# Kernel optimization log

Measured on AMD Instinct MI355X. Metric: run time of the kernel, lower is better.

Reference implementation:

```python
import jax, jax.numpy as jnp
import numpy as np

N, E, D, H = 16000, 256000, 128, 4
ALPHA = 0.2  # LeakyReLU negative slope


def setup_inputs() -> dict:
    key = jax.random.key(0)
    ks = jax.random.split(key, 9)
    s = 0.1
    return {
        "h": jax.random.normal(ks[0], (N, D), jnp.float32),
        "W": jax.random.normal(ks[1], (H, D, D), jnp.float32) * s,
        "a": jax.random.normal(ks[2], (H, 2 * D), jnp.float32) * s,
        "W_ih": jax.random.normal(ks[3], (3 * D, H * D), jnp.float32) * s,
        "W_hh": jax.random.normal(ks[4], (3 * D, D), jnp.float32) * s,
        "b_ih": jnp.zeros((3 * D,), jnp.float32),
        "b_hh": jnp.zeros((3 * D,), jnp.float32),
        "src": jax.random.randint(ks[5], (E,), 0, N, jnp.int32),
        "dst": jax.random.randint(ks[6], (E,), 0, N, jnp.int32),
    }


def reference(h, W, a, W_ih, W_hh, b_ih, b_hh, src, dst):
    n = h.shape[0]
    # Per-head linear transform: Wh[n,h,d]
    Wh = jnp.einsum("nd,hde->nhe", h, W)
    a1, a2 = a[:, :D], a[:, D:]
    s_src = jnp.einsum("nhd,hd->nh", Wh, a1)  # src attention logits
    s_dst = jnp.einsum("nhd,hd->nh", Wh, a2)  # dst attention logits
    e = jax.nn.leaky_relu(s_src[src] + s_dst[dst], ALPHA)  # [E,H]
    # Segment softmax over incoming edges of each dst node
    m = jax.ops.segment_max(e, dst, num_segments=n)          # [N,H]
    ex = jnp.exp(e - m[dst])
    denom = jax.ops.segment_sum(ex, dst, num_segments=n)     # [N,H]
    att = ex / denom[dst]                                    # [E,H]
    # Weighted message aggregation: h_prime[n,h,d]
    h_prime = jax.ops.segment_sum(att[:, :, None] * Wh[src], dst, num_segments=n)
    x = h_prime.reshape(n, H * D)  # concat heads
    # PyTorch GRUCell(input=H*D, hidden=D)
    gi = x @ W_ih.T + b_ih
    gh = h @ W_hh.T + b_hh
    i_r, i_z, i_n = jnp.split(gi, 3, axis=1)
    h_r, h_z, h_n = jnp.split(gh, 3, axis=1)
    r = jax.nn.sigmoid(i_r + h_r)
    z = jax.nn.sigmoid(i_z + h_z)
    nvec = jnp.tanh(i_n + r * h_n)
    return (1.0 - z) * nvec + z * h
```

## Files before the change

### kernel.cpp

```cpp
#include <hip/hip_runtime.h>
#include <math.h>

#define N_NODES 16000
#define E_EDGES 256000
#define DIM 128
#define HEADS 4
#define LRELU_ALPHA 0.2f
#define SLOT 64

typedef unsigned short u16;
typedef unsigned int u32;
typedef short bf16x8 __attribute__((ext_vector_type(8)));
typedef float floatx4 __attribute__((ext_vector_type(4)));

#define AS1 __attribute__((address_space(1)))
#define AS3 __attribute__((address_space(3)))

__device__ __forceinline__ u16 f2bf(float f) {
    u32 u = __float_as_uint(f);
    u32 r = (u + 0x7fffu + ((u >> 16) & 1u)) >> 16;
    return (u16)r;
}
__device__ __forceinline__ float bflo(u32 v) { return __uint_as_float(v << 16); }
__device__ __forceinline__ float bfhi(u32 v) { return __uint_as_float(v & 0xffff0000u); }
__device__ __forceinline__ u32 pack2(float lo, float hi) {
    return (u32)f2bf(lo) | ((u32)f2bf(hi) << 16);
}

__global__ __launch_bounds__(256) void prep_kernel(
    const float* __restrict__ hin, const float* __restrict__ W, const float* __restrict__ a,
    const float* __restrict__ W_ih, const float* __restrict__ W_hh,
    const int* __restrict__ src, const int* __restrict__ dst,
    u16* __restrict__ xcat, u16* __restrict__ Wihb, u16* __restrict__ Wb,
    u16* __restrict__ Wcat, float* __restrict__ wa1, float* __restrict__ wa2,
    u32* __restrict__ cnt, int* __restrict__ ssort)
{
    const int b = blockIdx.x;
    const int tid = threadIdx.x;
    if (b < 1000) {
        int e = b * 256 + tid;
        u32 base = cnt[N_NODES];
        int d = dst[e];
        u32 pos = atomicAdd(&cnt[d], 1u) - base;
        ssort[d * SLOT + pos] = src[e];
    } else if (b < 1768) {
        int i = (b - 1000) * 256 + tid;
        Wihb[i] = f2bf(W_ih[i]);
        if (i < HEADS * DIM * DIM) Wb[i] = f2bf(W[i]);
    } else if (b < 1960) {
        int t = (b - 1768) * 256 + tid;
        int jp = t >> 7, e = t & 127;
        int j = (jp < 256) ? jp : jp + 128;
        Wcat[(size_t)j * 640 + 512 + e] = f2bf(W_hh[jp * 128 + e]);
    } else if (b < 1962) {
        int t = (b - 1960) * 256 + tid;
        int h = t >> 7;
        const float* wrow = W + (long)t * DIM;
        const float* a1 = a + h * 2 * DIM;
        const float* a2 = a1 + DIM;
        float s1 = 0.f, s2 = 0.f;
        for (int e = 0; e < DIM; ++e) {
            float w = wrow[e];
            s1 = fmaf(w, a1[e], s1);
            s2 = fmaf(w, a2[e], s2);
        }
        wa1[t] = s1;
        wa2[t] = s2;
    } else {
        int p = (b - 1962) * 256 + tid;
        float2 hv = ((const float2*)hin)[p];
        ((u32*)xcat)[(p >> 6) * 320 + 256 + (p & 63)] = pack2(hv.x, hv.y);
    }
}

__device__ __forceinline__ void score_wave(int n, const float* __restrict__ hin,
    const float* __restrict__ wa1, const float* __restrict__ wa2,
    float* __restrict__ s_src, float* __restrict__ s_dst, int lane)
{
    float2 hv = ((const float2*)hin)[n * 64 + lane];
    float ps[4], qs[4];
    #pragma unroll
    for (int h = 0; h < 4; ++h) {
        float2 w1 = ((const float2*)(wa1 + h * 128))[lane];
        float2 w2 = ((const float2*)(wa2 + h * 128))[lane];
        float p = hv.x * w1.x + hv.y * w1.y;
        float q = hv.x * w2.x + hv.y * w2.y;
        #pragma unroll
        for (int off = 32; off > 0; off >>= 1) {
            p += __shfl_xor(p, off, 64);
            q += __shfl_xor(q, off, 64);
        }
        ps[h] = p; qs[h] = q;
    }
    if (lane == 0) {
        #pragma unroll
        for (int h = 0; h < 4; ++h) {
            s_src[n * HEADS + h] = ps[h];
            s_dst[n * HEADS + h] = qs[h];
        }
    }
}

__device__ __forceinline__ void gemm_tile(const u16* A, const u16* Bt, u16* C,
    int kstart, int kend, int lda, int ldb, int ldc, int row0, int col0, char* SMp, int tid)
{
    u16 (*Alds)[32] = (u16(*)[32])SMp;
    u16 (*Blds)[32] = (u16(*)[32])(SMp + 8192);
    const int wave = tid >> 6;
    const int lane = tid & 63;
    const int quad = lane >> 4;
    const int l15  = lane & 15;
    const int wm = (wave >> 1) * 64;
    const int wn = (wave & 1) * 64;
    const int ch0 = wave * 2;
    const int srow = lane >> 2;
    const int scol = (lane & 3) * 8;

    floatx4 acc[4][4] = {};

    for (int k0 = kstart; k0 < kend; k0 += 32) {
        #pragma unroll
        for (int c = 0; c < 2; ++c) {
            int ch = ch0 + c;
            const u16* ga = A + (size_t)(row0 + ch * 16 + srow) * lda + k0 + scol;
            __builtin_amdgcn_global_load_lds((AS1 void*)ga, (AS3 void*)&Alds[ch * 16][0], 16, 0, 0);
            const u16* gb = Bt + (size_t)(col0 + ch * 16 + srow) * ldb + k0 + scol;
            __builtin_amdgcn_global_load_lds((AS1 void*)gb, (AS3 void*)&Blds[ch * 16][0], 16, 0, 0);
        }
        __syncthreads();
        bf16x8 af[4], bfr[4];
        #pragma unroll
        for (int i = 0; i < 4; ++i) af[i] = *(const bf16x8*)&Alds[wm + i * 16 + l15][quad * 8];
        #pragma unroll
        for (int j = 0; j < 4; ++j) bfr[j] = *(const bf16x8*)&Blds[wn + j * 16 + l15][quad * 8];
        #pragma unroll
        for (int i = 0; i < 4; ++i)
            #pragma unroll
            for (int j = 0; j < 4; ++j)
                acc[i][j] = __builtin_amdgcn_mfma_f32_16x16x32_bf16(af[i], bfr[j], acc[i][j], 0, 0, 0);
        __syncthreads();
    }
    #pragma unroll
    for (int i = 0; i < 4; ++i) {
        #pragma unroll
        for (int r = 0; r < 4; ++r) {
            int row = row0 + wm + i * 16 + quad * 4 + r;
            size_t base = (size_t)row * ldc + col0 + wn + l15;
            #pragma unroll
            for (int j = 0; j < 4; ++j) C[base + j * 16] = f2bf(acc[i][j][r]);
        }
    }
}

__global__ __launch_bounds__(256) void mt_scores_kernel(
    const u16* __restrict__ Wihb, const u16* __restrict__ Wb, u16* __restrict__ Wcat,
    const float* __restrict__ hin, const float* __restrict__ wa1, const float* __restrict__ wa2,
    float* __restrict__ s_src, float* __restrict__ s_dst)
{
    __shared__ __align__(16) char SM[16384];
    const int tid = threadIdx.x;
    const int b = blockIdx.x;
    if (b < 12) {
        int y = b % 3, z = b / 3;
        gemm_tile(Wihb + z * 128, Wb + (size_t)z * 16384, Wcat + z * 128,
                  0, 128, 512, 128, 640, y * 128, 0, SM, tid);
    } else {
        for (int n = (b - 12) * 4 + (tid >> 6); n < N_NODES; n += 1024 * 4)
            score_wave(n, hin, wa1, wa2, s_src, s_dst, tid & 63);
    }
}

__global__ __launch_bounds__(256) void aggregate_kernel(
    const float* __restrict__ s_src, const float* __restrict__ s_dst,
    const u32* __restrict__ cnt, const int* __restrict__ srcs,
    u16* __restrict__ xcat)
{
    const int tid = threadIdx.x;
    const int lane = tid & 63;
    const int n = blockIdx.x * 4 + (tid >> 6);
    const u32 base = cnt[N_NODES];
    const int deg = (int)(cnt[n] - base);
    const int start = n * SLOT;
    u32* xrow = (u32*)(xcat + (size_t)n * 640);
    if (deg == 0) {
        #pragma unroll
        for (int h = 0; h < 4; ++h) xrow[h * 64 + lane] = 0u;
        return;
    }
    const u32* hb = (const u32*)xcat;
    const float sd = s_dst[n * HEADS + (lane & 3)];
    const int j16 = lane >> 2;
    const int hh  = lane & 3;

    float2 acc[4] = {{0.f,0.f},{0.f,0.f},{0.f,0.f},{0.f,0.f}};
    float dsum[4] = {0.f, 0.f, 0.f, 0.f};

    for (int cb = 0; cb < deg; cb += 16) {
        const int clen = min(16, deg - cb);
        int sv = 0;
        if (lane < clen) sv = srcs[start + cb + lane];
        float wv = 0.f;
        if (j16 < clen) {
            int s = __shfl(sv, j16, 64);
            float e = s_src[s * HEADS + hh] + sd;
            e = e > 0.f ? e : LRELU_ALPHA * e;
            wv = __expf(e);
        }
        int e = 0;
        for (; e + 8 <= clen; e += 8) {
            u32 vs[8];
            #pragma unroll
            for (int k = 0; k < 8; ++k) {
                int s = __shfl(sv, e + k, 64);
                vs[k] = hb[s * 320 + 256 + lane];
            }
            #pragma unroll
            for (int k = 0; k < 8; ++k) {
                float lo = bflo(vs[k]), hi = bfhi(vs[k]);
                #pragma unroll
                for (int h = 0; h < 4; ++h) {
                    float w = __shfl(wv, (e + k) * 4 + h, 64);
                    acc[h].x = fmaf(w, lo, acc[h].x);
                    acc[h].y = fmaf(w, hi, acc[h].y);
                    dsum[h] += w;
                }
            }
        }
        for (; e < clen; ++e) {
            int s = __shfl(sv, e, 64);
            u32 v = hb[s * 320 + 256 + lane];
            float lo = bflo(v), hi = bfhi(v);
            #pragma unroll
            for (int h = 0; h < 4; ++h) {
                float w = __shfl(wv, e * 4 + h, 64);
                acc[h].x = fmaf(w, lo, acc[h].x);
                acc[h].y = fmaf(w, hi, acc[h].y);
                dsum[h] += w;
            }
        }
    }
    #pragma unroll
    for (int h = 0; h < 4; ++h) {
        float invd = 1.f / dsum[h];
        xrow[h * 64 + lane] = pack2(acc[h].x * invd, acc[h].y * invd);
    }
}

__global__ __launch_bounds__(256) void gemm_main_kernel(
    const u16* __restrict__ xcat, const u16* __restrict__ Wcat, u16* __restrict__ g)
{
    __shared__ __align__(16) char SM[16384];
    const int x = blockIdx.x;
    const int ks = (x == 3) ? 512 : 0;
    const int ke = (x == 2) ? 512 : 640;
    gemm_tile(xcat, Wcat, g, ks, ke, 640, 640, 512,
              blockIdx.y * 128, x * 128, SM, threadIdx.x);
}

__global__ __launch_bounds__(256) void gru_kernel(const u32* __restrict__ g32,
    const float* __restrict__ b_ih, const float* __restrict__ b_hh,
    const float* __restrict__ hin, float* __restrict__ out)
{
    int p = blockIdx.x * 256 + threadIdx.x;
    if (p >= N_NODES * 64) return;
    int n = p >> 6, d2 = p & 63;
    const u32* gr = g32 + (size_t)n * 256;
    u32 vr = gr[d2], vz = gr[64 + d2], vi = gr[128 + d2], vh = gr[192 + d2];
    const float2* bi2 = (const float2*)b_ih;
    const float2* bh2 = (const float2*)b_hh;
    float2 bir = bi2[d2],       bhr = bh2[d2];
    float2 biz = bi2[64 + d2],  bhz = bh2[64 + d2];
    float2 bin = bi2[128 + d2], bhn = bh2[128 + d2];
    float2 hv = ((const float2*)hin)[p];
    float2 o;
    {
        float A = bflo(vr) + bir.x + bhr.x;
        float B = bflo(vz) + biz.x + bhz.x;
        float Cn = bflo(vi) + bin.x;
        float Dn = bflo(vh) + bhn.x;
        float r = 1.f / (1.f + __expf(-A));
        float z = 1.f / (1.f + __expf(-B));
        float e2 = __expf(2.f * (Cn + r * Dn));
        float nv = (e2 - 1.f) / (e2 + 1.f);
        o.x = (1.f - z) * nv + z * hv.x;
    }
    {
        float A = bfhi(vr) + bir.y + bhr.y;
        float B = bfhi(vz) + biz.y + bhz.y;
        float Cn = bfhi(vi) + bin.y;
        float Dn = bfhi(vh) + bhn.y;
        float r = 1.f / (1.f + __expf(-A));
        float z = 1.f / (1.f + __expf(-B));
        float e2 = __expf(2.f * (Cn + r * Dn));
        float nv = (e2 - 1.f) / (e2 + 1.f);
        o.y = (1.f - z) * nv + z * hv.y;
    }
    ((float2*)out)[p] = o;
}

extern "C" void kernel_launch(void* const* d_in, const int* in_sizes, int n_in,
                              void* d_out, int out_size, void* d_ws, size_t ws_size,
                              hipStream_t stream)
{
    const float* h    = (const float*)d_in[0];
    const float* W    = (const float*)d_in[1];
    const float* a    = (const float*)d_in[2];
    const float* W_ih = (const float*)d_in[3];
    const float* W_hh = (const float*)d_in[4];
    const float* b_ih = (const float*)d_in[5];
    const float* b_hh = (const float*)d_in[6];
    const int*   src  = (const int*)d_in[7];
    const int*   dst  = (const int*)d_in[8];
    float* out = (float*)d_out;

    char* ws = (char*)d_ws;
    size_t off = 0;
    auto alloc = [&](size_t bytes) { void* p = ws + off; off += (bytes + 255) & ~(size_t)255; return p; };

    u16*   xcat = (u16*)alloc((size_t)N_NODES * 640 * 2);
    u16*   g    = (u16*)alloc((size_t)N_NODES * 512 * 2);
    u16*   Wihb = (u16*)alloc(384 * 512 * 2);
    u16*   Wb   = (u16*)alloc(HEADS * DIM * DIM * 2);
    u16*   Wcat = (u16*)alloc(512 * 640 * 2);
    float* wa1  = (float*)alloc(512 * 4);
    float* wa2  = (float*)alloc(512 * 4);
    float* s_src = (float*)alloc((size_t)N_NODES * HEADS * 4);
    float* s_dst = (float*)alloc((size_t)N_NODES * HEADS * 4);
    u32*   cnt  = (u32*)alloc((N_NODES + 1) * 4);
    int*   ssort = (int*)alloc((size_t)N_NODES * SLOT * 4);

    prep_kernel<<<5962, 256, 0, stream>>>(
        h, W, a, W_ih, W_hh, src, dst, xcat, Wihb, Wb, Wcat, wa1, wa2, cnt, ssort);

    mt_scores_kernel<<<1036, 256, 0, stream>>>(
        Wihb, Wb, Wcat, h, wa1, wa2, s_src, s_dst);

    aggregate_kernel<<<N_NODES / 4, 256, 0, stream>>>(s_src, s_dst, cnt, ssort, xcat);

    gemm_main_kernel<<<dim3(4, 125), 256, 0, stream>>>(xcat, Wcat, g);

    gru_kernel<<<(N_NODES * 64 + 255) / 256, 256, 0, stream>>>(
        (const u32*)g, b_ih, b_hh, h, out);
}
```

Measured before the change: 152.2 us.

## Split main GEMM K range across two partial outputs and fuse h conversion into scores

The main GEMM grid gains a z dimension that splits each tile's K range in half. The two halves write separate bf16 partial buffers, which the GRU kernel loads and sums. This doubles the block count from 500 to 1000 so more CUs are busy, at the cost of extra partial-buffer traffic and an extra bf16 rounding step. The bf16 conversion of h into xcat also moves from prep_kernel into the score waves, which already load h, removing 4000 prep blocks and a redundant read of h.

```diff
diff --git a/kernel.cpp b/kernel.cpp
--- a/kernel.cpp
+++ b/kernel.cpp
@@ -28,10 +28,10 @@
 }
 
 __global__ __launch_bounds__(256) void prep_kernel(
-    const float* __restrict__ hin, const float* __restrict__ W, const float* __restrict__ a,
+    const float* __restrict__ W, const float* __restrict__ a,
     const float* __restrict__ W_ih, const float* __restrict__ W_hh,
     const int* __restrict__ src, const int* __restrict__ dst,
-    u16* __restrict__ xcat, u16* __restrict__ Wihb, u16* __restrict__ Wb,
+    u16* __restrict__ Wihb, u16* __restrict__ Wb,
     u16* __restrict__ Wcat, float* __restrict__ wa1, float* __restrict__ wa2,
     u32* __restrict__ cnt, int* __restrict__ ssort)
 {
@@ -52,7 +52,7 @@
         int jp = t >> 7, e = t & 127;
         int j = (jp < 256) ? jp : jp + 128;
         Wcat[(size_t)j * 640 + 512 + e] = f2bf(W_hh[jp * 128 + e]);
-    } else if (b < 1962) {
+    } else {
         int t = (b - 1960) * 256 + tid;
         int h = t >> 7;
         const float* wrow = W + (long)t * DIM;
@@ -66,18 +66,15 @@
         }
         wa1[t] = s1;
         wa2[t] = s2;
-    } else {
-        int p = (b - 1962) * 256 + tid;
-        float2 hv = ((const float2*)hin)[p];
-        ((u32*)xcat)[(p >> 6) * 320 + 256 + (p & 63)] = pack2(hv.x, hv.y);
     }
 }
 
 __device__ __forceinline__ void score_wave(int n, const float* __restrict__ hin,
     const float* __restrict__ wa1, const float* __restrict__ wa2,
-    float* __restrict__ s_src, float* __restrict__ s_dst, int lane)
+    float* __restrict__ s_src, float* __restrict__ s_dst, u16* __restrict__ xcat, int lane)
 {
     float2 hv = ((const float2*)hin)[n * 64 + lane];
+    ((u32*)xcat)[n * 320 + 256 + lane] = pack2(hv.x, hv.y);
     float ps[4], qs[4];
     #pragma unroll
     for (int h = 0; h < 4; ++h) {
@@ -155,7 +152,7 @@
 __global__ __launch_bounds__(256) void mt_scores_kernel(
     const u16* __restrict__ Wihb, const u16* __restrict__ Wb, u16* __restrict__ Wcat,
     const float* __restrict__ hin, const float* __restrict__ wa1, const float* __restrict__ wa2,
-    float* __restrict__ s_src, float* __restrict__ s_dst)
+    float* __restrict__ s_src, float* __restrict__ s_dst, u16* __restrict__ xcat)
 {
     __shared__ __align__(16) char SM[16384];
     const int tid = threadIdx.x;
@@ -166,7 +163,7 @@
                   0, 128, 512, 128, 640, y * 128, 0, SM, tid);
     } else {
         for (int n = (b - 12) * 4 + (tid >> 6); n < N_NODES; n += 1024 * 4)
-            score_wave(n, hin, wa1, wa2, s_src, s_dst, tid & 63);
+            score_wave(n, hin, wa1, wa2, s_src, s_dst, xcat, tid & 63);
     }
 }
 
@@ -251,9 +248,13 @@
 {
     __shared__ __align__(16) char SM[16384];
     const int x = blockIdx.x;
-    const int ks = (x == 3) ? 512 : 0;
-    const int ke = (x == 2) ? 512 : 640;
-    gemm_tile(xcat, Wcat, g, ks, ke, 640, 640, 512,
+    const int ks0 = (x == 3) ? 512 : 0;
+    const int ke0 = (x == 2) ? 512 : 640;
+    const int mid = (ks0 + ke0) >> 1;
+    const int ks = blockIdx.z ? mid : ks0;
+    const int ke = blockIdx.z ? ke0 : mid;
+    u16* gp = g + (size_t)blockIdx.z * N_NODES * 512;
+    gemm_tile(xcat, Wcat, gp, ks, ke, 640, 640, 512,
               blockIdx.y * 128, x * 128, SM, threadIdx.x);
 }
 
@@ -264,8 +265,12 @@
     int p = blockIdx.x * 256 + threadIdx.x;
     if (p >= N_NODES * 64) return;
     int n = p >> 6, d2 = p & 63;
-    const u32* gr = g32 + (size_t)n * 256;
-    u32 vr = gr[d2], vz = gr[64 + d2], vi = gr[128 + d2], vh = gr[192 + d2];
+    const u32* gr0 = g32 + (size_t)n * 256;
+    const u32* gr1 = gr0 + (size_t)N_NODES * 256;
+    u32 ar = gr0[d2],       br = gr1[d2];
+    u32 az = gr0[64 + d2],  bz = gr1[64 + d2];
+    u32 ai = gr0[128 + d2], bi = gr1[128 + d2];
+    u32 ah = gr0[192 + d2], bh = gr1[192 + d2];
     const float2* bi2 = (const float2*)b_ih;
     const float2* bh2 = (const float2*)b_hh;
     float2 bir = bi2[d2],       bhr = bh2[d2];
@@ -274,10 +279,10 @@
     float2 hv = ((const float2*)hin)[p];
     float2 o;
     {
-        float A = bflo(vr) + bir.x + bhr.x;
-        float B = bflo(vz) + biz.x + bhz.x;
-        float Cn = bflo(vi) + bin.x;
-        float Dn = bflo(vh) + bhn.x;
+        float A = bflo(ar) + bflo(br) + bir.x + bhr.x;
+        float B = bflo(az) + bflo(bz) + biz.x + bhz.x;
+        float Cn = bflo(ai) + bflo(bi) + bin.x;
+        float Dn = bflo(ah) + bflo(bh) + bhn.x;
         float r = 1.f / (1.f + __expf(-A));
         float z = 1.f / (1.f + __expf(-B));
         float e2 = __expf(2.f * (Cn + r * Dn));
@@ -285,10 +290,10 @@
         o.x = (1.f - z) * nv + z * hv.x;
     }
     {
-        float A = bfhi(vr) + bir.y + bhr.y;
-        float B = bfhi(vz) + biz.y + bhz.y;
-        float Cn = bfhi(vi) + bin.y;
-        float Dn = bfhi(vh) + bhn.y;
+        float A = bfhi(ar) + bfhi(br) + bir.y + bhr.y;
+        float B = bfhi(az) + bfhi(bz) + biz.y + bhz.y;
+        float Cn = bfhi(ai) + bfhi(bi) + bin.y;
+        float Dn = bfhi(ah) + bfhi(bh) + bhn.y;
         float r = 1.f / (1.f + __expf(-A));
         float z = 1.f / (1.f + __expf(-B));
         float e2 = __expf(2.f * (Cn + r * Dn));
@@ -318,7 +323,7 @@
     auto alloc = [&](size_t bytes) { void* p = ws + off; off += (bytes + 255) & ~(size_t)255; return p; };
 
     u16*   xcat = (u16*)alloc((size_t)N_NODES * 640 * 2);
-    u16*   g    = (u16*)alloc((size_t)N_NODES * 512 * 2);
+    u16*   g    = (u16*)alloc((size_t)N_NODES * 512 * 2 * 2);
     u16*   Wihb = (u16*)alloc(384 * 512 * 2);
     u16*   Wb   = (u16*)alloc(HEADS * DIM * DIM * 2);
     u16*   Wcat = (u16*)alloc(512 * 640 * 2);
@@ -329,15 +334,15 @@
     u32*   cnt  = (u32*)alloc((N_NODES + 1) * 4);
     int*   ssort = (int*)alloc((size_t)N_NODES * SLOT * 4);
 
-    prep_kernel<<<5962, 256, 0, stream>>>(
-        h, W, a, W_ih, W_hh, src, dst, xcat, Wihb, Wb, Wcat, wa1, wa2, cnt, ssort);
+    prep_kernel<<<1962, 256, 0, stream>>>(
+        W, a, W_ih, W_hh, src, dst, Wihb, Wb, Wcat, wa1, wa2, cnt, ssort);
 
     mt_scores_kernel<<<1036, 256, 0, stream>>>(
-        Wihb, Wb, Wcat, h, wa1, wa2, s_src, s_dst);
+        Wihb, Wb, Wcat, h, wa1, wa2, s_src, s_dst, xcat);
 
     aggregate_kernel<<<N_NODES / 4, 256, 0, stream>>>(s_src, s_dst, cnt, ssort, xcat);
 
-    gemm_main_kernel<<<dim3(4, 125), 256, 0, stream>>>(xcat, Wcat, g);
+    gemm_main_kernel<<<dim3(4, 125, 2), 256, 0, stream>>>(xcat, Wcat, g);
 
     gru_kernel<<<(N_NODES * 64 + 255) / 256, 256, 0, stream>>>(
         (const u32*)g, b_ih, b_hh, h, out);
```

Result: no change. 153.4 us (+0.8%).
